# Performance work log

Measured on AMD Instinct MI355X. Metric: run time of the kernel, lower is better.

Reference implementation:

```python
import jax, jax.numpy as jnp
import numpy as np

N = 50000
E = 1600000
IN_C = 64
TIME_DIM = 32
HID = 32
HEADS = 4
OUT_C = 2
MAX_TIME = 50
NEG_SLOPE = 0.2


def setup_inputs() -> dict:
    key = jax.random.key(0)
    ks = jax.random.split(key, 16)
    in_dim = IN_C + TIME_DIM          # 96
    d1 = HEADS * HID                  # 128
    inp = {
        "x": jax.random.normal(ks[0], (N, IN_C), dtype=jnp.float32),
        "edge_index": jax.random.randint(ks[1], (2, E), 0, N, dtype=jnp.int32),
        "time_step": jax.random.randint(ks[2], (N,), 0, MAX_TIME + 1, dtype=jnp.int32),
        "W_time": jax.random.normal(ks[3], (MAX_TIME + 1, TIME_DIM), dtype=jnp.float32) * 0.1,
        # layer 0: GATv2(in_dim -> HID, heads=HEADS, concat=True)
        "W_l0": jax.random.normal(ks[4], (in_dim, d1), dtype=jnp.float32) * (1.0 / np.sqrt(in_dim)),
        "b_l0": jnp.zeros((d1,), dtype=jnp.float32),
        "W_r0": jax.random.normal(ks[5], (in_dim, d1), dtype=jnp.float32) * (1.0 / np.sqrt(in_dim)),
        "b_r0": jnp.zeros((d1,), dtype=jnp.float32),
        "att0": jax.random.normal(ks[6], (HEADS, HID), dtype=jnp.float32) * (1.0 / np.sqrt(HID)),
        "bias0": jnp.zeros((d1,), dtype=jnp.float32),
        # layer 1: GATv2(d1 -> OUT_C, heads=1, concat=False)
        "W_l1": jax.random.normal(ks[7], (d1, OUT_C), dtype=jnp.float32) * (1.0 / np.sqrt(d1)),
        "b_l1": jnp.zeros((OUT_C,), dtype=jnp.float32),
        "W_r1": jax.random.normal(ks[8], (d1, OUT_C), dtype=jnp.float32) * (1.0 / np.sqrt(d1)),
        "b_r1": jnp.zeros((OUT_C,), dtype=jnp.float32),
        "att1": jax.random.normal(ks[9], (1, OUT_C), dtype=jnp.float32) * (1.0 / np.sqrt(OUT_C)),
        "bias1": jnp.zeros((OUT_C,), dtype=jnp.float32),
    }
    return inp


def _gatv2(h, src, dst, Wl, bl, Wr, br, att, bias, heads, out_c, concat):
    # PyG GATv2Conv (share_weights=False, eval mode, add_self_loops already done)
    xl = (h @ Wl + bl).reshape(-1, heads, out_c)   # source transform
    xr = (h @ Wr + br).reshape(-1, heads, out_c)   # target transform
    e = xl[src] + xr[dst]                          # [E', H, C]
    logit = jnp.einsum('ehc,hc->eh', jax.nn.leaky_relu(e, NEG_SLOPE), att)
    m = jax.ops.segment_max(logit, dst, num_segments=N)       # segment-softmax
    a = jnp.exp(logit - m[dst])
    s = jax.ops.segment_sum(a, dst, num_segments=N)
    alpha = a / (s[dst] + 1e-16)                   # [E', H]
    out = jax.ops.segment_sum(alpha[:, :, None] * xl[src], dst, num_segments=N)
    out = out.reshape(N, heads * out_c) if concat else out.mean(axis=1)
    return out + bias


def reference(x, edge_index, time_step, W_time,
              W_l0, b_l0, W_r0, b_r0, att0, bias0,
              W_l1, b_l1, W_r1, b_r1, att1, bias1):
    # add self loops (PyG default add_self_loops=True)
    loops = jnp.arange(N, dtype=edge_index.dtype)
    src = jnp.concatenate([edge_index[0], loops])
    dst = jnp.concatenate([edge_index[1], loops])

    t = W_time[time_step]                          # [N, time_dim]
    h = jnp.concatenate([x, t], axis=1)            # [N, in_dim]

    h = _gatv2(h, src, dst, W_l0, b_l0, W_r0, b_r0, att0, bias0, HEADS, HID, True)
    h = jax.nn.relu(h)                             # dropout off (eval)
    h = _gatv2(h, src, dst, W_l1, b_l1, W_r1, b_r1, att1, bias1, 1, OUT_C, False)
    return h
```

## Files before the change

### kernel.cpp

```cpp
#include <hip/hip_runtime.h>
#include <hip/hip_fp16.h>

#define NN 50000
#define NE 1600000
#define EP (NE + NN)
#define INC 64
#define TDIM 32
#define INDIM 96
#define D1 128
#define NEG 0.2f
#define LOG2E 1.44269504f

#define CBSH 8
#define NCB 196
#define GCAP 9600
#define TILE 8192

#define MT 64
#define KP 104

typedef _Float16 h2v __attribute__((ext_vector_type(2)));
typedef _Float16 f16x8 __attribute__((ext_vector_type(8)));
typedef float f32x4 __attribute__((ext_vector_type(4)));
union H2U { unsigned u; __half2 h; h2v v; };

__device__ __forceinline__ float lrelu(float v) { return v > 0.f ? v : NEG * v; }

__global__ __launch_bounds__(256) void k_wcast(
    const float* __restrict__ Wl, const float* __restrict__ Wr,
    const float* __restrict__ bl, const float* __restrict__ br,
    __half* __restrict__ Btg, float* __restrict__ bcat)
{
    int idx = blockIdx.x * 256 + threadIdx.x;
    if (idx < 256) bcat[idx] = (idx < 128) ? bl[idx] : br[idx - 128];
    if (idx >= 256 * INDIM) return;
    int c = idx / INDIM, k = idx - c * INDIM;
    float v = (c < 128) ? Wl[k * D1 + c] : Wr[k * D1 + (c - 128)];
    Btg[idx] = __float2half(v);
}

__global__ __launch_bounds__(256) void k_gemm0m(
    const float* __restrict__ x, const int* __restrict__ ts,
    const float* __restrict__ Wt,
    const __half* __restrict__ Btg, const float* __restrict__ bcat,
    __half* __restrict__ xl0, __half* __restrict__ xr0)
{
    __shared__ _Float16 As[MT][KP];
    const int t = threadIdx.x;
    const int base = blockIdx.x * MT;
    const float4* __restrict__ x4  = reinterpret_cast<const float4*>(x);
    const float4* __restrict__ wt4 = reinterpret_cast<const float4*>(Wt);

    const int lane = t & 63;
    const int w = t >> 6;
    const int lo4 = lane & 15;
    const int hi2 = lane >> 4;

    f16x8 bfr[3][4];
#pragma unroll
    for (int ks = 0; ks < 3; ++ks)
#pragma unroll
        for (int ns = 0; ns < 4; ++ns)
            bfr[ks][ns] = *reinterpret_cast<const f16x8*>(
                Btg + (size_t)(w * 64 + ns * 16 + lo4) * INDIM + ks * 32 + hi2 * 8);

    float4 av0, av1, av2, av3, av4, av5;
#define LOADA(J, AV)                                                   \
    {   int c = t + (J) * 256;                                         \
        int m = c / 24, q = c - m * 24;                                \
        int n = base + m;                                              \
        if (n < NN)                                                    \
            AV = (q < 16) ? x4[(size_t)n * 16 + q]                     \
                          : wt4[(size_t)ts[n] * 8 + (q - 16)];         \
        else AV = make_float4(0.f, 0.f, 0.f, 0.f);                     \
    }
    LOADA(0, av0) LOADA(1, av1) LOADA(2, av2)
    LOADA(3, av3) LOADA(4, av4) LOADA(5, av5)
#undef LOADA
#define WRITEA(J, AV)                                                  \
    {   int c = t + (J) * 256;                                         \
        int m = c / 24, q = c - m * 24;                                \
        h2v p01 = { (_Float16)AV.x, (_Float16)AV.y };                  \
        h2v p23 = { (_Float16)AV.z, (_Float16)AV.w };                  \
        *reinterpret_cast<h2v*>(&As[m][q * 4])     = p01;              \
        *reinterpret_cast<h2v*>(&As[m][q * 4 + 2]) = p23;              \
    }
    WRITEA(0, av0) WRITEA(1, av1) WRITEA(2, av2)
    WRITEA(3, av3) WRITEA(4, av4) WRITEA(5, av5)
#undef WRITEA
    __syncthreads();

    f32x4 acc[4][4] = {};
#pragma unroll
    for (int ks = 0; ks < 3; ++ks) {
        const int kb = ks * 32 + hi2 * 8;
        f16x8 a[4];
#pragma unroll
        for (int ms = 0; ms < 4; ++ms)
            a[ms] = *reinterpret_cast<const f16x8*>(&As[ms * 16 + lo4][kb]);
#pragma unroll
        for (int ms = 0; ms < 4; ++ms)
#pragma unroll
            for (int ns = 0; ns < 4; ++ns)
                acc[ms][ns] = __builtin_amdgcn_mfma_f32_16x16x32_f16(
                    a[ms], bfr[ks][ns], acc[ms][ns], 0, 0, 0);
    }

#pragma unroll
    for (int ms = 0; ms < 4; ++ms) {
#pragma unroll
        for (int ns = 0; ns < 4; ++ns) {
            int col = w * 64 + ns * 16 + lo4;
            float bv = bcat[col];
            __half* outp = (col & 128) ? xr0 : xl0;
            int cc = col & 127;
#pragma unroll
            for (int r = 0; r < 4; ++r) {
                int node = base + ms * 16 + hi2 * 4 + r;
                if (node < NN)
                    outp[(size_t)node * D1 + cc] = __float2half(acc[ms][ns][r] + bv);
            }
        }
    }
}

__global__ __launch_bounds__(1024) void k_part(
    const int* __restrict__ ei, int* __restrict__ gcnt, unsigned* __restrict__ cstage)
{
    __shared__ int cnt[NCB], loff[NCB + 1], gbasel[NCB], lpos[NCB];
    __shared__ unsigned pay[TILE];
    const int t = threadIdx.x;
    const int ntiles = (EP + TILE - 1) / TILE;
    for (int tile = blockIdx.x; tile < ntiles; tile += gridDim.x) {
        const int tb = tile * TILE;
        const int tc = min(TILE, EP - tb);
        if (t < NCB) cnt[t] = 0;
        __syncthreads();
        unsigned pk0, pk1, pk2, pk3, pk4, pk5, pk6, pk7;
#define LOADK(K, PK)                                              \
        {   int i = t + (K) * 1024;                               \
            if (i < tc) {                                         \
                int e = tb + i; int s, d;                         \
                if (e < NE) { s = ei[e]; d = ei[NE + e]; }        \
                else        { s = e - NE; d = s; }                \
                PK = ((unsigned)d << 16) | (unsigned)s;           \
                atomicAdd(&cnt[d >> CBSH], 1);                    \
            } }
        LOADK(0, pk0) LOADK(1, pk1) LOADK(2, pk2) LOADK(3, pk3)
        LOADK(4, pk4) LOADK(5, pk5) LOADK(6, pk6) LOADK(7, pk7)
#undef LOADK
        __syncthreads();
        if (t == 0) {
            int run = 0;
            for (int b = 0; b < NCB; ++b) { loff[b] = run; run += cnt[b]; }
            loff[NCB] = run;
        }
        __syncthreads();
        if (t < NCB) {
            gbasel[t] = atomicAdd(&gcnt[t], cnt[t]);
            lpos[t] = loff[t];
        }
        __syncthreads();
#define PLACEK(K, PK)                                             \
        {   int i = t + (K) * 1024;                               \
            if (i < tc) {                                         \
                int cb = (int)(PK >> (16 + CBSH));                \
                int p = atomicAdd(&lpos[cb], 1);                  \
                pay[p] = PK;                                      \
            } }
        PLACEK(0, pk0) PLACEK(1, pk1) PLACEK(2, pk2) PLACEK(3, pk3)
        PLACEK(4, pk4) PLACEK(5, pk5) PLACEK(6, pk6) PLACEK(7, pk7)
#undef PLACEK
        __syncthreads();
        for (int j = t; j < tc; j += 1024) {
            unsigned v = pay[j];
            int cb = (int)(v >> (16 + CBSH));
            int pos = gbasel[cb] + (j - loff[cb]);
            if (pos < GCAP) cstage[(size_t)cb * GCAP + pos] = v;
        }
        __syncthreads();
    }
}

__global__ void k_cscan(const int* __restrict__ gcnt, int* __restrict__ gbase,
                        int* __restrict__ rowst)
{
    if (threadIdx.x == 0) {
        int run = 0;
        for (int b = 0; b < NCB; ++b) { gbase[b] = run; run += min(gcnt[b], GCAP); }
        rowst[NN] = run;
    }
}

__global__ __launch_bounds__(1024) void k_build2(
    const int* __restrict__ gcnt, const int* __restrict__ gbase,
    const unsigned* __restrict__ cstage,
    int* __restrict__ rowst, unsigned short* __restrict__ csr)
{
    const int b = blockIdx.x;
    const int t = threadIdx.x;
    __shared__ int hist[256], sc[256], curs[256];
    const int cnt = min(gcnt[b], GCAP);
    const int base = gbase[b];
    const int d0 = b << CBSH;
    const int nd = min(256, NN - d0);
    if (t < 256) hist[t] = 0;
    __syncthreads();
    const unsigned* __restrict__ src = cstage + (size_t)b * GCAP;
    for (int i = t; i < cnt; i += 1024)
        atomicAdd(&hist[(src[i] >> 16) & 255], 1);
    __syncthreads();
    if (t < 256) sc[t] = hist[t];
    __syncthreads();
    for (int off = 1; off < 256; off <<= 1) {
        int v = 0;
        if (t < 256 && t >= off) v = sc[t - off];
        __syncthreads();
        if (t < 256) sc[t] += v;
        __syncthreads();
    }
    if (t < 256) {
        int excl = sc[t] - hist[t];
        curs[t] = excl;
        if (t < nd) rowst[d0 + t] = base + excl;
    }
    __syncthreads();
    for (int i = t; i < cnt; i += 1024) {
        unsigned v = src[i];
        int p = atomicAdd(&curs[(v >> 16) & 255], 1);
        csr[base + p] = (unsigned short)(v & 0xFFFFu);
    }
}

__global__ __launch_bounds__(256) void k_agg0(
    const int* __restrict__ rowst, const unsigned short* __restrict__ csr,
    const __half* __restrict__ xl0, const __half* __restrict__ xr0,
    const float* __restrict__ att0, const float* __restrict__ bias0,
    const float* __restrict__ Wl1, const float* __restrict__ bl1,
    const float* __restrict__ Wr1, const float* __restrict__ br1,
    float* __restrict__ xl1, float* __restrict__ xr1)
{
    const int d = (blockIdx.x * 256 + threadIdx.x) >> 6;
    const int lane = threadIdx.x & 63;
    if (d >= NN) return;
    const int slot  = lane >> 4;
    const int lane4 = lane & 15;
    const int c0 = lane4 * 8;

    uint4 xrw = *reinterpret_cast<const uint4*>(xr0 + (size_t)d * D1 + c0);
    H2U xr01, xr23, xr45, xr67;
    xr01.u = xrw.x; xr23.u = xrw.y; xr45.u = xrw.z; xr67.u = xrw.w;
    float4 atf0 = *reinterpret_cast<const float4*>(att0 + c0);
    float4 atf1 = *reinterpret_cast<const float4*>(att0 + c0 + 4);
    H2U at01, at23, at45, at67;
    at01.h = __floats2half2_rn(atf0.x * LOG2E, atf0.y * LOG2E);
    at23.h = __floats2half2_rn(atf0.z * LOG2E, atf0.w * LOG2E);
    at45.h = __floats2half2_rn(atf1.x * LOG2E, atf1.y * LOG2E);
    at67.h = __floats2half2_rn(atf1.z * LOG2E, atf1.w * LOG2E);
    const _Float16 kneg = (_Float16)NEG;
    const h2v k2 = { kneg, kneg };

    const int rs = rowst[d];
    const int cnt = rowst[d + 1] - rs;
    h2v a01 = {(_Float16)0.f, (_Float16)0.f};
    h2v a23 = a01, a45 = a01, a67 = a01;
    float wsum = 0.f;

#define EDGE(W, VALID)                                                      \
    {   H2U x01, x23, x45, x67;                                             \
        x01.u = (W).x; x23.u = (W).y; x45.u = (W).z; x67.u = (W).w;         \
        h2v s01 = x01.v + xr01.v, s23 = x23.v + xr23.v;                     \
        h2v s45 = x45.v + xr45.v, s67 = x67.v + xr67.v;                     \
        h2v l01 = __builtin_elementwise_max(s01, s01 * k2);                 \
        h2v l23 = __builtin_elementwise_max(s23, s23 * k2);                 \
        h2v l45 = __builtin_elementwise_max(s45, s45 * k2);                 \
        h2v l67 = __builtin_elementwise_max(s67, s67 * k2);                 \
        float p = __builtin_amdgcn_fdot2(l01, at01.v,                       \
                  __builtin_amdgcn_fdot2(l23, at23.v,                       \
                  __builtin_amdgcn_fdot2(l45, at45.v,                       \
                  __builtin_amdgcn_fdot2(l67, at67.v, 0.f, false),          \
                  false), false), false);                                   \
        p += __shfl_xor(p, 1);                                              \
        p += __shfl_xor(p, 2);                                              \
        float wgt = (VALID) ? exp2f(p) : 0.f;                               \
        _Float16 wh = (_Float16)wgt;                                        \
        h2v w2 = { wh, wh };                                                \
        a01 = __builtin_elementwise_fma(w2, x01.v, a01);                    \
        a23 = __builtin_elementwise_fma(w2, x23.v, a23);                    \
        a45 = __builtin_elementwise_fma(w2, x45.v, a45);                    \
        a67 = __builtin_elementwise_fma(w2, x67.v, a67);                    \
        wsum += wgt;                                                        \
    }

    int i = 0;
    if (cnt >= 8) {
        int s0 = csr[rs + slot];
        int s1 = csr[rs + 4 + slot];
        for (; i + 8 <= cnt; i += 8) {
            uint4 w0 = *reinterpret_cast<const uint4*>(xl0 + (size_t)s0 * D1 + c0);
            uint4 w1 = *reinterpret_cast<const uint4*>(xl0 + (size_t)s1 * D1 + c0);
            if (i + 16 <= cnt) {
                s0 = csr[rs + i + 8 + slot];
                s1 = csr[rs + i + 12 + slot];
            }
            EDGE(w0, true);
            EDGE(w1, true);
        }
    }
    for (; i < cnt; i += 4) {
        int e = i + slot;
        bool valid = (e < cnt);
        int s = csr[rs + (valid ? e : 0)];
        uint4 w = *reinterpret_cast<const uint4*>(xl0 + (size_t)s * D1 + c0);
        EDGE(w, valid);
    }
#undef EDGE

    H2U u01, u23, u45, u67;
    u01.v = a01; u23.v = a23; u45.v = a45; u67.v = a67;
    float2 f01 = __half22float2(u01.h), f23 = __half22float2(u23.h);
    float2 f45 = __half22float2(u45.h), f67 = __half22float2(u67.h);
    float acc0 = f01.x, acc1 = f01.y, acc2 = f23.x, acc3 = f23.y;
    float acc4 = f45.x, acc5 = f45.y, acc6 = f67.x, acc7 = f67.y;

#define COMB(V) V += __shfl_xor(V, 16); V += __shfl_xor(V, 32);
    COMB(acc0) COMB(acc1) COMB(acc2) COMB(acc3)
    COMB(acc4) COMB(acc5) COMB(acc6) COMB(acc7)
    COMB(wsum)
#undef COMB

    if (slot == 0) {
        float r = 1.f / (wsum + 1e-16f);
        float4 b0 = *reinterpret_cast<const float4*>(bias0 + c0);
        float4 b1 = *reinterpret_cast<const float4*>(bias0 + c0 + 4);
        float h[8];
        h[0] = fmaxf(acc0 * r + b0.x, 0.f);
        h[1] = fmaxf(acc1 * r + b0.y, 0.f);
        h[2] = fmaxf(acc2 * r + b0.z, 0.f);
        h[3] = fmaxf(acc3 * r + b0.w, 0.f);
        h[4] = fmaxf(acc4 * r + b1.x, 0.f);
        h[5] = fmaxf(acc5 * r + b1.y, 0.f);
        h[6] = fmaxf(acc6 * r + b1.z, 0.f);
        h[7] = fmaxf(acc7 * r + b1.w, 0.f);
        float pl0 = 0.f, pl1 = 0.f, pr0 = 0.f, pr1 = 0.f;
#pragma unroll
        for (int j = 0; j < 8; ++j) {
            float2 wl = *reinterpret_cast<const float2*>(Wl1 + (c0 + j) * 2);
            float2 wr = *reinterpret_cast<const float2*>(Wr1 + (c0 + j) * 2);
            pl0 += h[j] * wl.x; pl1 += h[j] * wl.y;
            pr0 += h[j] * wr.x; pr1 += h[j] * wr.y;
        }
#pragma unroll
        for (int ofs = 1; ofs < 16; ofs <<= 1) {
            pl0 += __shfl_xor(pl0, ofs);
            pl1 += __shfl_xor(pl1, ofs);
            pr0 += __shfl_xor(pr0, ofs);
            pr1 += __shfl_xor(pr1, ofs);
        }
        if (lane4 == 0) {
            *reinterpret_cast<float2*>(xl1 + (size_t)d * 2) =
                make_float2(pl0 + bl1[0], pl1 + bl1[1]);
            *reinterpret_cast<float2*>(xr1 + (size_t)d * 2) =
                make_float2(pr0 + br1[0], pr1 + br1[1]);
        }
    }
}

__global__ __launch_bounds__(256) void k_layer1(
    const int* __restrict__ rowst, const unsigned short* __restrict__ csr,
    const float* __restrict__ xl1, const float* __restrict__ xr1,
    const float* __restrict__ att1, const float* __restrict__ bias1,
    float* __restrict__ out)
{
    const int d = (blockIdx.x * 256 + threadIdx.x) >> 2;
    const int sub = threadIdx.x & 3;
    if (d >= NN) return;
    float2 xr = *reinterpret_cast<const float2*>(xr1 + (size_t)d * 2);
    float A0 = att1[0], A1 = att1[1];
    const int rs = rowst[d], re = rowst[d + 1];
    float sum = 0.f, a0 = 0.f, a1 = 0.f;
    for (int i = rs + sub; i < re; i += 4) {
        int s = csr[i];
        float2 xs = *reinterpret_cast<const float2*>(xl1 + (size_t)s * 2);
        float wgt = __expf(lrelu(xs.x + xr.x) * A0 + lrelu(xs.y + xr.y) * A1);
        sum += wgt;
        a0 += wgt * xs.x;
        a1 += wgt * xs.y;
    }
    sum += __shfl_xor(sum, 1); sum += __shfl_xor(sum, 2);
    a0  += __shfl_xor(a0, 1);  a0  += __shfl_xor(a0, 2);
    a1  += __shfl_xor(a1, 1);  a1  += __shfl_xor(a1, 2);
    if (sub == 0) {
        float r = 1.f / (sum + 1e-16f);
        out[(size_t)d * 2]     = a0 * r + bias1[0];
        out[(size_t)d * 2 + 1] = a1 * r + bias1[1];
    }
}

extern "C" void kernel_launch(void* const* d_in, const int* in_sizes, int n_in,
                              void* d_out, int out_size, void* d_ws, size_t ws_size,
                              hipStream_t stream)
{
    const float* x     = (const float*)d_in[0];
    const int*   ei    = (const int*)d_in[1];
    const int*   ts    = (const int*)d_in[2];
    const float* Wt    = (const float*)d_in[3];
    const float* Wl0   = (const float*)d_in[4];
    const float* bl0   = (const float*)d_in[5];
    const float* Wr0   = (const float*)d_in[6];
    const float* br0   = (const float*)d_in[7];
    const float* att0  = (const float*)d_in[8];
    const float* bias0 = (const float*)d_in[9];
    const float* Wl1   = (const float*)d_in[10];
    const float* bl1   = (const float*)d_in[11];
    const float* Wr1   = (const float*)d_in[12];
    const float* br1   = (const float*)d_in[13];
    const float* att1  = (const float*)d_in[14];
    const float* bias1 = (const float*)d_in[15];
    float* out = (float*)d_out;

    char* wsp = (char*)d_ws;
    size_t off = 0;
    auto alloc = [&](size_t bytes) -> void* {
        void* p = wsp + off;
        off += (bytes + 255) & ~(size_t)255;
        return p;
    };
    __half* xl0  = (__half*)alloc((size_t)NN * D1 * 2);
    __half* xr0  = (__half*)alloc((size_t)NN * D1 * 2);
    float* xl1   = (float*)alloc((size_t)NN * 2 * 4);
    float* xr1   = (float*)alloc((size_t)NN * 2 * 4);
    int* rowst   = (int*)alloc((size_t)(NN + 1) * 4);
    unsigned short* csr = (unsigned short*)alloc((size_t)EP * 2);
    int* gcnt        = (int*)alloc((size_t)NCB * 4);
    int* gbase       = (int*)alloc((size_t)NCB * 4);
    unsigned* cstage = (unsigned*)alloc((size_t)NCB * GCAP * 4);
    __half* Btg      = (__half*)alloc((size_t)256 * INDIM * 2);
    float* bcat      = (float*)alloc((size_t)256 * 4);

    k_wcast<<<(256 * INDIM + 255) / 256, 256, 0, stream>>>(Wl0, Wr0, bl0, br0, Btg, bcat);
    k_gemm0m<<<(NN + MT - 1) / MT, 256, 0, stream>>>(x, ts, Wt, Btg, bcat, xl0, xr0);

    (void)hipMemsetAsync(gcnt, 0, (size_t)NCB * 4, stream);
    const int ntiles = (EP + TILE - 1) / TILE;
    k_part<<<ntiles, 1024, 0, stream>>>(ei, gcnt, cstage);
    k_cscan<<<1, 64, 0, stream>>>(gcnt, gbase, rowst);
    k_build2<<<NCB, 1024, 0, stream>>>(gcnt, gbase, cstage, rowst, csr);

    k_agg0<<<(NN + 3) / 4, 256, 0, stream>>>(rowst, csr, xl0, xr0, att0, bias0,
                                             Wl1, bl1, Wr1, br1, xl1, xr1);
    k_layer1<<<(NN * 4 + 255) / 256, 256, 0, stream>>>(rowst, csr, xl1, xr1, att1, bias1, out);
}
```

Before: 139.3 us.

## Fuse layer-0 GEMM and edge partition into one interleaved kernel launch

Merges the MFMA projection GEMM and the edge-bucketing partition kernel into a single launch. Even blocks do GEMM tiles and odd blocks do partition tiles, which now use 256 threads and 2048-edge tiles. The two phases share one LDS union. The aim is to overlap compute-bound GEMM work with memory- and atomic-bound partition work, and to remove a launch. In exchange, more partition tiles mean more global atomics on the bucket counters, and LDS sizing is set by the larger union member.

```diff
diff --git a/kernel.cpp b/kernel.cpp
--- a/kernel.cpp
+++ b/kernel.cpp
@@ -14,10 +14,12 @@
 #define CBSH 8
 #define NCB 196
 #define GCAP 9600
-#define TILE 8192
+#define PTILE 2048
 
 #define MT 64
 #define KP 104
+#define NGEMM ((NN + MT - 1) / MT)
+#define NPTILES ((EP + PTILE - 1) / PTILE)
 
 typedef _Float16 h2v __attribute__((ext_vector_type(2)));
 typedef _Float16 f16x8 __attribute__((ext_vector_type(8)));
@@ -39,146 +41,151 @@
     Btg[idx] = __float2half(v);
 }
 
-__global__ __launch_bounds__(256) void k_gemm0m(
+__global__ __launch_bounds__(256) void k_g0p(
     const float* __restrict__ x, const int* __restrict__ ts,
     const float* __restrict__ Wt,
     const __half* __restrict__ Btg, const float* __restrict__ bcat,
-    __half* __restrict__ xl0, __half* __restrict__ xr0)
-{
-    __shared__ _Float16 As[MT][KP];
+    __half* __restrict__ xl0, __half* __restrict__ xr0,
+    const int* __restrict__ ei, int* __restrict__ gcnt,
+    unsigned* __restrict__ cstage)
+{
+    __shared__ union SH {
+        _Float16 As[MT][KP];
+        struct {
+            int cnt[NCB], loff[NCB + 1], gbasel[NCB], lpos[NCB];
+            unsigned pay[PTILE];
+        } p;
+    } sh;
     const int t = threadIdx.x;
-    const int base = blockIdx.x * MT;
-    const float4* __restrict__ x4  = reinterpret_cast<const float4*>(x);
-    const float4* __restrict__ wt4 = reinterpret_cast<const float4*>(Wt);
-
-    const int lane = t & 63;
-    const int w = t >> 6;
-    const int lo4 = lane & 15;
-    const int hi2 = lane >> 4;
-
-    f16x8 bfr[3][4];
-#pragma unroll
-    for (int ks = 0; ks < 3; ++ks)
-#pragma unroll
-        for (int ns = 0; ns < 4; ++ns)
-            bfr[ks][ns] = *reinterpret_cast<const f16x8*>(
-                Btg + (size_t)(w * 64 + ns * 16 + lo4) * INDIM + ks * 32 + hi2 * 8);
-
-    float4 av0, av1, av2, av3, av4, av5;
+    const int half = blockIdx.x >> 1;
+
+    if ((blockIdx.x & 1) == 0) {
+        if (half >= NGEMM) return;
+        const int base = half * MT;
+        const float4* __restrict__ x4  = reinterpret_cast<const float4*>(x);
+        const float4* __restrict__ wt4 = reinterpret_cast<const float4*>(Wt);
+
+        const int lane = t & 63;
+        const int w = t >> 6;
+        const int lo4 = lane & 15;
+        const int hi2 = lane >> 4;
+
+        f16x8 bfr[3][4];
+#pragma unroll
+        for (int ks = 0; ks < 3; ++ks)
+#pragma unroll
+            for (int ns = 0; ns < 4; ++ns)
+                bfr[ks][ns] = *reinterpret_cast<const f16x8*>(
+                    Btg + (size_t)(w * 64 + ns * 16 + lo4) * INDIM + ks * 32 + hi2 * 8);
+
+        float4 av0, av1, av2, av3, av4, av5;
 #define LOADA(J, AV)                                                   \
-    {   int c = t + (J) * 256;                                         \
-        int m = c / 24, q = c - m * 24;                                \
-        int n = base + m;                                              \
-        if (n < NN)                                                    \
-            AV = (q < 16) ? x4[(size_t)n * 16 + q]                     \
-                          : wt4[(size_t)ts[n] * 8 + (q - 16)];         \
-        else AV = make_float4(0.f, 0.f, 0.f, 0.f);                     \
-    }
-    LOADA(0, av0) LOADA(1, av1) LOADA(2, av2)
-    LOADA(3, av3) LOADA(4, av4) LOADA(5, av5)
+        {   int c = t + (J) * 256;                                     \
+            int m = c / 24, q = c - m * 24;                            \
+            int n = base + m;                                          \
+            if (n < NN)                                                \
+                AV = (q < 16) ? x4[(size_t)n * 16 + q]                 \
+                              : wt4[(size_t)ts[n] * 8 + (q - 16)];     \
+            else AV = make_float4(0.f, 0.f, 0.f, 0.f);                 \
+        }
+        LOADA(0, av0) LOADA(1, av1) LOADA(2, av2)
+        LOADA(3, av3) LOADA(4, av4) LOADA(5, av5)
 #undef LOADA
 #define WRITEA(J, AV)                                                  \
-    {   int c = t + (J) * 256;                                         \
-        int m = c / 24, q = c - m * 24;                                \
-        h2v p01 = { (_Float16)AV.x, (_Float16)AV.y };                  \
-        h2v p23 = { (_Float16)AV.z, (_Float16)AV.w };                  \
-        *reinterpret_cast<h2v*>(&As[m][q * 4])     = p01;              \
-        *reinterpret_cast<h2v*>(&As[m][q * 4 + 2]) = p23;              \
-    }
-    WRITEA(0, av0) WRITEA(1, av1) WRITEA(2, av2)
-    WRITEA(3, av3) WRITEA(4, av4) WRITEA(5, av5)
+        {   int c = t + (J) * 256;                                     \
+            int m = c / 24, q = c - m * 24;                            \
+            h2v p01 = { (_Float16)AV.x, (_Float16)AV.y };              \
+            h2v p23 = { (_Float16)AV.z, (_Float16)AV.w };              \
+            *reinterpret_cast<h2v*>(&sh.As[m][q * 4])     = p01;       \
+            *reinterpret_cast<h2v*>(&sh.As[m][q * 4 + 2]) = p23;       \
+        }
+        WRITEA(0, av0) WRITEA(1, av1) WRITEA(2, av2)
+        WRITEA(3, av3) WRITEA(4, av4) WRITEA(5, av5)
 #undef WRITEA
-    __syncthreads();
-
-    f32x4 acc[4][4] = {};
-#pragma unroll
-    for (int ks = 0; ks < 3; ++ks) {
-        const int kb = ks * 32 + hi2 * 8;
-        f16x8 a[4];
-#pragma unroll
-        for (int ms = 0; ms < 4; ++ms)
-            a[ms] = *reinterpret_cast<const f16x8*>(&As[ms * 16 + lo4][kb]);
-#pragma unroll
-        for (int ms = 0; ms < 4; ++ms)
-#pragma unroll
-            for (int ns = 0; ns < 4; ++ns)
-                acc[ms][ns] = __builtin_amdgcn_mfma_f32_16x16x32_f16(
-                    a[ms], bfr[ks][ns], acc[ms][ns], 0, 0, 0);
-    }
-
-#pragma unroll
-    for (int ms = 0; ms < 4; ++ms) {
-#pragma unroll
-        for (int ns = 0; ns < 4; ++ns) {
-            int col = w * 64 + ns * 16 + lo4;
-            float bv = bcat[col];
-            __half* outp = (col & 128) ? xr0 : xl0;
-            int cc = col & 127;
-#pragma unroll
-            for (int r = 0; r < 4; ++r) {
-                int node = base + ms * 16 + hi2 * 4 + r;
-                if (node < NN)
-                    outp[(size_t)node * D1 + cc] = __float2half(acc[ms][ns][r] + bv);
+        __syncthreads();
+
+        f32x4 acc[4][4] = {};
+#pragma unroll
+        for (int ks = 0; ks < 3; ++ks) {
+            const int kb = ks * 32 + hi2 * 8;
+            f16x8 a[4];
+#pragma unroll
+            for (int ms = 0; ms < 4; ++ms)
+                a[ms] = *reinterpret_cast<const f16x8*>(&sh.As[ms * 16 + lo4][kb]);
+#pragma unroll
+            for (int ms = 0; ms < 4; ++ms)
+#pragma unroll
+                for (int ns = 0; ns < 4; ++ns)
+                    acc[ms][ns] = __builtin_amdgcn_mfma_f32_16x16x32_f16(
+                        a[ms], bfr[ks][ns], acc[ms][ns], 0, 0, 0);
+        }
+
+#pragma unroll
+        for (int ms = 0; ms < 4; ++ms) {
+#pragma unroll
+            for (int ns = 0; ns < 4; ++ns) {
+                int col = w * 64 + ns * 16 + lo4;
+                float bv = bcat[col];
+                __half* outp = (col & 128) ? xr0 : xl0;
+                int cc = col & 127;
+#pragma unroll
+                for (int r = 0; r < 4; ++r) {
+                    int node = base + ms * 16 + hi2 * 4 + r;
+                    if (node < NN)
+                        outp[(size_t)node * D1 + cc] = __float2half(acc[ms][ns][r] + bv);
+                }
             }
         }
-    }
-}
-
-__global__ __launch_bounds__(1024) void k_part(
-    const int* __restrict__ ei, int* __restrict__ gcnt, unsigned* __restrict__ cstage)
-{
-    __shared__ int cnt[NCB], loff[NCB + 1], gbasel[NCB], lpos[NCB];
-    __shared__ unsigned pay[TILE];
-    const int t = threadIdx.x;
-    const int ntiles = (EP + TILE - 1) / TILE;
-    for (int tile = blockIdx.x; tile < ntiles; tile += gridDim.x) {
-        const int tb = tile * TILE;
-        const int tc = min(TILE, EP - tb);
-        if (t < NCB) cnt[t] = 0;
-        __syncthreads();
-        unsigned pk0, pk1, pk2, pk3, pk4, pk5, pk6, pk7;
+    } else {
+        for (int tile = half; tile < NPTILES; tile += (gridDim.x >> 1)) {
+            const int tb = tile * PTILE;
+            const int tc = min(PTILE, EP - tb);
+            if (t < NCB) sh.p.cnt[t] = 0;
+            __syncthreads();
+            unsigned pk0, pk1, pk2, pk3, pk4, pk5, pk6, pk7;
 #define LOADK(K, PK)                                              \
-        {   int i = t + (K) * 1024;                               \
-            if (i < tc) {                                         \
-                int e = tb + i; int s, d;                         \
-                if (e < NE) { s = ei[e]; d = ei[NE + e]; }        \
-                else        { s = e - NE; d = s; }                \
-                PK = ((unsigned)d << 16) | (unsigned)s;           \
-                atomicAdd(&cnt[d >> CBSH], 1);                    \
-            } }
-        LOADK(0, pk0) LOADK(1, pk1) LOADK(2, pk2) LOADK(3, pk3)
-        LOADK(4, pk4) LOADK(5, pk5) LOADK(6, pk6) LOADK(7, pk7)
+            {   int i = t + (K) * 256;                            \
+                if (i < tc) {                                     \
+                    int e = tb + i; int s, d;                     \
+                    if (e < NE) { s = ei[e]; d = ei[NE + e]; }    \
+                    else        { s = e - NE; d = s; }            \
+                    PK = ((unsigned)d << 16) | (unsigned)s;       \
+                    atomicAdd(&sh.p.cnt[d >> CBSH], 1);           \
+                } }
+            LOADK(0, pk0) LOADK(1, pk1) LOADK(2, pk2) LOADK(3, pk3)
+            LOADK(4, pk4) LOADK(5, pk5) LOADK(6, pk6) LOADK(7, pk7)
 #undef LOADK
-        __syncthreads();
-        if (t == 0) {
-            int run = 0;
-            for (int b = 0; b < NCB; ++b) { loff[b] = run; run += cnt[b]; }
-            loff[NCB] = run;
-        }
-        __syncthreads();
-        if (t < NCB) {
-            gbasel[t] = atomicAdd(&gcnt[t], cnt[t]);
-            lpos[t] = loff[t];
-        }
-        __syncthreads();
+            __syncthreads();
+            if (t == 0) {
+                int run = 0;
+                for (int b = 0; b < NCB; ++b) { sh.p.loff[b] = run; run += sh.p.cnt[b]; }
+                sh.p.loff[NCB] = run;
+            }
+            __syncthreads();
+            if (t < NCB) {
+                sh.p.gbasel[t] = atomicAdd(&gcnt[t], sh.p.cnt[t]);
+                sh.p.lpos[t] = sh.p.loff[t];
+            }
+            __syncthreads();
 #define PLACEK(K, PK)                                             \
-        {   int i = t + (K) * 1024;                               \
-            if (i < tc) {                                         \
-                int cb = (int)(PK >> (16 + CBSH));                \
-                int p = atomicAdd(&lpos[cb], 1);                  \
-                pay[p] = PK;                                      \
-            } }
-        PLACEK(0, pk0) PLACEK(1, pk1) PLACEK(2, pk2) PLACEK(3, pk3)
-        PLACEK(4, pk4) PLACEK(5, pk5) PLACEK(6, pk6) PLACEK(7, pk7)
+            {   int i = t + (K) * 256;                            \
+                if (i < tc) {                                     \
+                    int cb = (int)(PK >> (16 + CBSH));            \
+                    int p = atomicAdd(&sh.p.lpos[cb], 1);         \
+                    sh.p.pay[p] = PK;                             \
+                } }
+            PLACEK(0, pk0) PLACEK(1, pk1) PLACEK(2, pk2) PLACEK(3, pk3)
+            PLACEK(4, pk4) PLACEK(5, pk5) PLACEK(6, pk6) PLACEK(7, pk7)
 #undef PLACEK
-        __syncthreads();
-        for (int j = t; j < tc; j += 1024) {
-            unsigned v = pay[j];
-            int cb = (int)(v >> (16 + CBSH));
-            int pos = gbasel[cb] + (j - loff[cb]);
-            if (pos < GCAP) cstage[(size_t)cb * GCAP + pos] = v;
-        }
-        __syncthreads();
+            __syncthreads();
+            for (int j = t; j < tc; j += 256) {
+                unsigned v = sh.p.pay[j];
+                int cb = (int)(v >> (16 + CBSH));
+                int pos = sh.p.gbasel[cb] + (j - sh.p.loff[cb]);
+                if (pos < GCAP) cstage[(size_t)cb * GCAP + pos] = v;
+            }
+            __syncthreads();
+        }
     }
 }
 
@@ -438,12 +445,12 @@
     __half* Btg      = (__half*)alloc((size_t)256 * INDIM * 2);
     float* bcat      = (float*)alloc((size_t)256 * 4);
 
+    (void)hipMemsetAsync(gcnt, 0, (size_t)NCB * 4, stream);
     k_wcast<<<(256 * INDIM + 255) / 256, 256, 0, stream>>>(Wl0, Wr0, bl0, br0, Btg, bcat);
-    k_gemm0m<<<(NN + MT - 1) / MT, 256, 0, stream>>>(x, ts, Wt, Btg, bcat, xl0, xr0);
-
-    (void)hipMemsetAsync(gcnt, 0, (size_t)NCB * 4, stream);
-    const int ntiles = (EP + TILE - 1) / TILE;
-    k_part<<<ntiles, 1024, 0, stream>>>(ei, gcnt, cstage);
+
+    const int nfused = 2 * ((NGEMM > NPTILES) ? NGEMM : NPTILES);
+    k_g0p<<<nfused, 256, 0, stream>>>(x, ts, Wt, Btg, bcat, xl0, xr0, ei, gcnt, cstage);
+
     k_cscan<<<1, 64, 0, stream>>>(gcnt, gbase, rowst);
     k_build2<<<NCB, 1024, 0, stream>>>(gcnt, gbase, cstage, rowst, csr);
 
```

Result: faster. 133.5 us (-4.2%).
